# Performance work log

Hardware: AMD Instinct MI355X
Metric: run time of the kernel (lower is better)

## Reference

```python
import jax, jax.numpy as jnp
import numpy as np
import math

B, T, E, H, QL, SUB = 4, 2048, 64, 8, 6, 64  # batch, win_len, n_embd, n_head, q_len, sub_len


def _row_mask(index, sub_len, win_len):
    log_l = math.ceil(np.log2(sub_len))
    mask = np.zeros(win_len, dtype=np.float32)
    if (win_len // sub_len) * 2 * log_l > index:
        mask[: index + 1] = 1
    else:
        while index >= 0:
            if index - log_l + 1 < 0:
                mask[:index] = 1
                break
            mask[index - log_l + 1 : index + 1] = 1
            for i in range(log_l):
                new_index = index - log_l + 1 - 2 ** i
                if index - new_index <= sub_len and new_index >= 0:
                    mask[new_index] = 1
            index -= sub_len
    return mask


def _log_mask(win_len, sub_len):
    m = np.zeros((win_len, win_len), dtype=np.float32)
    for i in range(win_len):
        m[i] = _row_mask(i, sub_len, win_len)
    return m.reshape(1, 1, win_len, win_len)


def setup_inputs() -> dict:
    key = jax.random.key(0)
    ks = jax.random.split(key, 4)
    x = jax.random.normal(ks[0], (B, T, E), dtype=jnp.float32)
    Wqk = jax.random.normal(ks[1], (2 * H * E, E, QL), dtype=jnp.float32) * 0.02
    bqk = jnp.zeros((2 * H * E,), dtype=jnp.float32)
    Wv = jax.random.normal(ks[2], (E, H * E), dtype=jnp.float32) * 0.02
    bv = jnp.zeros((H * E,), dtype=jnp.float32)
    Wp = jax.random.normal(ks[3], (H * E, E), dtype=jnp.float32) * 0.02
    bp = jnp.zeros((E,), dtype=jnp.float32)
    mask = jnp.asarray(_log_mask(T, SUB).astype(bool))  # [1,1,T,T] bool
    return {"x": x, "Wqk": Wqk, "bqk": bqk, "Wv": Wv, "bv": bv,
            "Wp": Wp, "bp": bp, "mask": mask}


def reference(x, Wqk, bqk, Wv, bv, Wp, bp, mask):
    b, t, e = x.shape
    h = Wv.shape[1] // e
    ql = Wqk.shape[-1]

    # value projection (Conv1D rf=1 == dense)
    value = x @ Wv + bv                              # [B,T,H*E]

    # causal conv1d QK projection: left-pad by q_len-1
    xc = jnp.transpose(x, (0, 2, 1))                 # [B,E,T]
    qk = jax.lax.conv_general_dilated(
        xc, Wqk, window_strides=(1,), padding=[(ql - 1, 0)],
        dimension_numbers=("NCH", "OIH", "NCH"))    # [B,2*H*E,T]
    qk = qk + bqk[None, :, None]
    qk = jnp.transpose(qk, (0, 2, 1))                # [B,T,2*H*E]
    query, key_ = jnp.split(qk, 2, axis=2)

    q = query.reshape(b, t, h, e).transpose(0, 2, 1, 3)   # [B,H,T,E]
    k = key_.reshape(b, t, h, e).transpose(0, 2, 3, 1)    # [B,H,E,T]
    v = value.reshape(b, t, h, e).transpose(0, 2, 1, 3)   # [B,H,T,E]

    pre = jnp.einsum("bhqe,bhek->bhqk", q, k) / jnp.sqrt(jnp.asarray(e, x.dtype))
    m = mask[:, :, :t, :t].astype(pre.dtype)
    pre = pre * m + (-1e9) * (1.0 - m)
    attn_weights = jax.nn.softmax(pre, axis=-1)           # [B,H,T,T]
    # dropout p=0.0 -> identity
    attn = jnp.einsum("bhqk,bhke->bhqe", attn_weights, v)  # [B,H,T,E]
    attn = attn.transpose(0, 2, 1, 3).reshape(b, t, h * e)
    out = attn @ Wp + bp                                  # [B,T,E]
    return out, attn_weights
```

## Files before the change

kernel.cpp:

```cpp
#include <hip/hip_runtime.h>
#include <hip/hip_bf16.h>


typedef __attribute__((ext_vector_type(8))) short bf16x8;
typedef __attribute__((ext_vector_type(4))) float f32x4;
typedef unsigned int uint32;

#define MFMA16(a, b, c) __builtin_amdgcn_mfma_f32_16x16x32_bf16((a), (b), (c), 0, 0, 0)

static __device__ __forceinline__ bool sparse_pred(int r, int c) {
  int d = r - c;
  if (d < 0) return false;
  int o = d & 63;
  int j = c + o;
  bool inS = (o <= 7) || (o == 9) || (o == 13) || (o == 21) || (o == 37);
  return (j >= 5) ? inS : (o >= 1);
}

static __device__ __forceinline__ uint32 bfbits(float x) {
  __hip_bfloat16 h = __float2bfloat16(x);
  unsigned short u;
  __builtin_memcpy(&u, &h, 2);
  return (uint32)u;
}

static __device__ __forceinline__ unsigned pred4(bool causal, int ct, int rt, int q, int nt,
                                                 int lq, const unsigned* pm4) {
  const int tb = ct * 64 + 16 * nt + 4 * lq;
  const int thr = q - tb;
  const unsigned cb = (thr < 0) ? 0u : (thr >= 3 ? 0xFu : (0xFu >> (3 - thr)));
  if (causal) return (ct < rt) ? 0xFu : cb;
  if (ct == 0) {
    unsigned p = 0;
#pragma unroll
    for (int reg = 0; reg < 4; ++reg) p |= (unsigned)sparse_pred(q, tb + reg) << reg;
    return p;
  }
  unsigned p = pm4[nt];
  if (ct == rt) p &= cb;
  return p;
}

struct KF {
  bf16x8 a[8];
};

static __device__ __forceinline__ KF loadK(const __hip_bfloat16* __restrict__ kbh, int ct, int lm,
                                           int lq) {
  KF f;
  const __hip_bfloat16* kbase = kbh + (size_t)ct * 64 * 64;
#pragma unroll
  for (int nb = 0; nb < 4; ++nb) {
    const __hip_bfloat16* krow = kbase + (size_t)(16 * nb + lm) * 64;
    f.a[2 * nb] = *reinterpret_cast<const bf16x8*>(krow + lq * 8);
    f.a[2 * nb + 1] = *reinterpret_cast<const bf16x8*>(krow + 32 + lq * 8);
  }
  return f;
}

struct VF {
  bf16x8 a[8];
};

static __device__ __forceinline__ VF loadV(const __hip_bfloat16* __restrict__ vbh, int ct, int lm,
                                           int lq) {
  VF f;
  const __hip_bfloat16* vbase = vbh + ct * 64;
#pragma unroll
  for (int eb = 0; eb < 4; ++eb) {
    const __hip_bfloat16* vrow = vbase + (size_t)(16 * eb + lm) * 2048;
    f.a[2 * eb] = *reinterpret_cast<const bf16x8*>(vrow + lq * 8);
    f.a[2 * eb + 1] = *reinterpret_cast<const bf16x8*>(vrow + 32 + lq * 8);
  }
  return f;
}

__global__ void prep_kernel(const float* __restrict__ Wqk, const float* __restrict__ Wv,
                            __hip_bfloat16* __restrict__ Wt_qk, __hip_bfloat16* __restrict__ Wv_t) {
  int idx = blockIdx.x * 256 + threadIdx.x;
  if (idx < 1024 * 384) {
    int o = idx / 384, kidx = idx - o * 384;
    int kk = kidx >> 6, i = kidx & 63;
    Wt_qk[idx] = __float2bfloat16(Wqk[(o * 64 + i) * 6 + kk]);
  } else {
    int j = idx - 1024 * 384;
    int n = j >> 6, k = j & 63;
    Wv_t[j] = __float2bfloat16(Wv[k * 512 + n]);
  }
}

__global__ __launch_bounds__(256, 4) void proj_kernel(
    const float* __restrict__ x, const float* __restrict__ bqk, const float* __restrict__ bv,
    const __hip_bfloat16* __restrict__ Wt_qk, const __hip_bfloat16* __restrict__ Wv_t,
    __hip_bfloat16* __restrict__ q_bf, __hip_bfloat16* __restrict__ k_bf,
    __hip_bfloat16* __restrict__ v_bf) {
  const int tokTile = blockIdx.x;
  const int chTile = blockIdx.y;
  const int gt0 = tokTile * 64;
  const int b = gt0 >> 11;
  const int t0 = gt0 & 2047;
  const int thr = threadIdx.x;
  __shared__ __align__(16) __hip_bfloat16 xwin[69][72];
  __shared__ __align__(16) __hip_bfloat16 vt[64][72];

  for (int u = thr; u < 69 * 64; u += 256) {
    int row = u >> 6, i = u & 63;
    int t = t0 - 5 + row;
    float v = (t >= 0) ? x[((size_t)b * 2048 + t) * 64 + i] : 0.f;
    xwin[row][i] = __float2bfloat16(v);
  }
  __syncthreads();

  const int wave = thr >> 6, lane = thr & 63;
  const int lm = lane & 15, lq = lane >> 4;
  f32x4 acc[4];
#pragma unroll
  for (int nb = 0; nb < 4; ++nb) acc[nb] = (f32x4){0.f, 0.f, 0.f, 0.f};

  if (chTile < 16) {
    const int ch0 = chTile * 64;
    for (int kc = 0; kc < 12; ++kc) {
      int k0 = kc * 32 + lq * 8;
      int kk = k0 >> 6, i0 = k0 & 63;
      bf16x8 a = *reinterpret_cast<const bf16x8*>(&xwin[16 * wave + lm + kk][i0]);
#pragma unroll
      for (int nb = 0; nb < 4; ++nb) {
        bf16x8 bb =
            *reinterpret_cast<const bf16x8*>(&Wt_qk[(size_t)(ch0 + 16 * nb + lm) * 384 + k0]);
        acc[nb] = MFMA16(a, bb, acc[nb]);
      }
    }
#pragma unroll
    for (int nb = 0; nb < 4; ++nb) {
      int e = 16 * nb + lm;
      float bias = bqk[chTile * 64 + e];
#pragma unroll
      for (int reg = 0; reg < 4; ++reg)
        vt[16 * wave + lq * 4 + reg][e] = __float2bfloat16(acc[nb][reg] + bias);
    }
    __syncthreads();
    const int half = (chTile >> 3) & 1;
    const int h = chTile & 7;
    __hip_bfloat16* dst = half ? k_bf : q_bf;
    for (int u = thr; u < 512; u += 256) {
      int row = u >> 3, c8 = u & 7;
      *reinterpret_cast<uint4*>(dst + ((size_t)((b * 8 + h) * 2048 + t0 + row)) * 64 + c8 * 8) =
          *reinterpret_cast<const uint4*>(&vt[row][c8 * 8]);
    }
  } else {
    const int nv0 = (chTile - 16) * 64;
    for (int kc = 0; kc < 2; ++kc) {
      int i0 = kc * 32 + lq * 8;
      bf16x8 a = *reinterpret_cast<const bf16x8*>(&xwin[16 * wave + lm + 5][i0]);
#pragma unroll
      for (int nb = 0; nb < 4; ++nb) {
        bf16x8 bb = *reinterpret_cast<const bf16x8*>(&Wv_t[(size_t)(nv0 + 16 * nb + lm) * 64 + i0]);
        acc[nb] = MFMA16(a, bb, acc[nb]);
      }
    }
#pragma unroll
    for (int nb = 0; nb < 4; ++nb) {
      int e = 16 * nb + lm;
      float bias = bv[nv0 + e];
#pragma unroll
      for (int reg = 0; reg < 4; ++reg)
        vt[e][16 * wave + lq * 4 + reg] = __float2bfloat16(acc[nb][reg] + bias);
    }
    __syncthreads();
    const int h = chTile - 16;
    for (int u = thr; u < 512; u += 256) {
      int e = u >> 3, c8 = u & 7;
      *reinterpret_cast<uint4*>(v_bf + ((size_t)((b * 8 + h) * 64 + e)) * 2048 + t0 + c8 * 8) =
          *reinterpret_cast<const uint4*>(&vt[e][c8 * 8]);
    }
  }
}

__global__ __launch_bounds__(256, 2) void attn_kernel(
    const __hip_bfloat16* __restrict__ q_bf, const __hip_bfloat16* __restrict__ k_bf,
    const __hip_bfloat16* __restrict__ v_bf,
    float* __restrict__ attn, float* __restrict__ attnout) {
  const int bh = blockIdx.y;
  const int wave = threadIdx.x >> 6;
  const int lane = threadIdx.x & 63;
  const int lm = lane & 15, lq = lane >> 4;

  __shared__ __align__(16) __hip_bfloat16 psw[4][16 * 72];
  __hip_bfloat16* pw = psw[wave];

  const int b2 = bh >> 3, h = bh & 7;
  const __hip_bfloat16* kbh = k_bf + (size_t)bh * 2048 * 64;
  const __hip_bfloat16* vbh = v_bf + (size_t)bh * 64 * 2048;

  const int q64 = 16 * wave + lm;
  unsigned pm4[4];
  {
    const int S[12] = {0, 1, 2, 3, 4, 5, 6, 7, 9, 13, 21, 37};
    unsigned long long M = 0;
#pragma unroll
    for (int i = 0; i < 12; ++i) M |= 1ull << ((q64 - S[i]) & 63);
#pragma unroll
    for (int nt = 0; nt < 4; ++nt) pm4[nt] = (unsigned)((M >> (16 * nt + 4 * lq)) & 0xFull);
  }

  for (int task = 0; task < 2; ++task) {
    const int rt = (task == 0) ? (int)blockIdx.x : 31 - (int)blockIdx.x;
    const int r0 = rt * 64;
    const bool causal = (rt < 6);
    const int q = r0 + q64;

    const __hip_bfloat16* qrow = q_bf + ((size_t)bh * 2048 + q) * 64;
    bf16x8 qa0 = *reinterpret_cast<const bf16x8*>(qrow + lq * 8);
    bf16x8 qa1 = *reinterpret_cast<const bf16x8*>(qrow + 32 + lq * 8);

    float lsum = 0.f;
    {
      KF kc = loadK(kbh, 0, lm, lq);
      for (int ct = 0; ct <= rt; ++ct) {
        KF kn = kc;
        if (ct < rt) kn = loadK(kbh, ct + 1, lm, lq);
#pragma unroll
        for (int nt = 0; nt < 4; ++nt) {
          f32x4 c = (f32x4){0.f, 0.f, 0.f, 0.f};
          c = MFMA16(kc.a[2 * nt], qa0, c);
          c = MFMA16(kc.a[2 * nt + 1], qa1, c);
          const unsigned p = pred4(causal, ct, rt, q, nt, lq, pm4);
#pragma unroll
          for (int reg = 0; reg < 4; ++reg)
            lsum += ((p >> reg) & 1u) ? __expf(c[reg] * 0.125f) : 0.f;
        }
        kc = kn;
      }
    }
    lsum += __shfl_xor(lsum, 16);
    lsum += __shfl_xor(lsum, 32);
    const float inv = 1.f / lsum;

    f32x4 oacc[4];
#pragma unroll
    for (int eb = 0; eb < 4; ++eb) oacc[eb] = (f32x4){0.f, 0.f, 0.f, 0.f};
    float* aq = attn + ((size_t)bh * 2048 + q) * 2048;

    KF kc = loadK(kbh, 0, lm, lq);
    for (int ct = 0; ct <= rt; ++ct) {
      VF vf = loadV(vbh, ct, lm, lq);
      KF kn = kc;
      if (ct < rt) kn = loadK(kbh, ct + 1, lm, lq);
#pragma unroll
      for (int nt = 0; nt < 4; ++nt) {
        f32x4 c = (f32x4){0.f, 0.f, 0.f, 0.f};
        c = MFMA16(kc.a[2 * nt], qa0, c);
        c = MFMA16(kc.a[2 * nt + 1], qa1, c);
        const unsigned p = pred4(causal, ct, rt, q, nt, lq, pm4);
        f32x4 w;
#pragma unroll
        for (int reg = 0; reg < 4; ++reg)
          w[reg] = ((p >> reg) & 1u) ? __expf(c[reg] * 0.125f) * inv : 0.f;
        *reinterpret_cast<f32x4*>(aq + ct * 64 + 16 * nt + 4 * lq) = w;
        uint32 u0 = bfbits(w[0]) | (bfbits(w[1]) << 16);
        uint32 u1 = bfbits(w[2]) | (bfbits(w[3]) << 16);
        uint2 uu = {u0, u1};
        *reinterpret_cast<uint2*>(&pw[lm * 72 + 16 * nt + 4 * lq]) = uu;
      }
      bf16x8 pa0 = *reinterpret_cast<const bf16x8*>(&pw[lm * 72 + lq * 8]);
      bf16x8 pa1 = *reinterpret_cast<const bf16x8*>(&pw[lm * 72 + 32 + lq * 8]);
#pragma unroll
      for (int eb = 0; eb < 4; ++eb) {
        oacc[eb] = MFMA16(vf.a[2 * eb], pa0, oacc[eb]);
        oacc[eb] = MFMA16(vf.a[2 * eb + 1], pa1, oacc[eb]);
      }
      kc = kn;
    }

    float* oq = attnout + ((size_t)(b2 * 2048 + q)) * 512 + h * 64;
#pragma unroll
    for (int eb = 0; eb < 4; ++eb)
      *reinterpret_cast<f32x4*>(oq + 16 * eb + 4 * lq) = oacc[eb];
  }
}

__global__ __launch_bounds__(256, 4) void outproj_kernel(const float* __restrict__ attnout,
                                                         const float* __restrict__ Wp,
                                                         const float* __restrict__ bp,
                                                         float* __restrict__ out) {
  __shared__ __align__(16) float wp_s[128][64];
  const int thr = threadIdx.x;
  const int wave = thr >> 6, lane = thr & 63;
  const int row0 = blockIdx.x * 16 + wave * 4;
  float acc[4] = {0.f, 0.f, 0.f, 0.f};
  for (int kt = 0; kt < 4; ++kt) {
    __syncthreads();
    for (int u = thr; u < 2048; u += 256) {
      int r = u >> 4, c4 = (u & 15) * 4;
      *reinterpret_cast<float4*>(&wp_s[r][c4]) =
          *reinterpret_cast<const float4*>(&Wp[(size_t)(kt * 128 + r) * 64 + c4]);
    }
    __syncthreads();
    for (int k4 = 0; k4 < 32; ++k4) {
      float wv0 = wp_s[k4 * 4 + 0][lane];
      float wv1 = wp_s[k4 * 4 + 1][lane];
      float wv2 = wp_s[k4 * 4 + 2][lane];
      float wv3 = wp_s[k4 * 4 + 3][lane];
#pragma unroll
      for (int rr = 0; rr < 4; ++rr) {
        const float4 a = *reinterpret_cast<const float4*>(
            &attnout[(size_t)(row0 + rr) * 512 + kt * 128 + k4 * 4]);
        acc[rr] += a.x * wv0 + a.y * wv1 + a.z * wv2 + a.w * wv3;
      }
    }
  }
  const float bias = bp[lane];
#pragma unroll
  for (int rr = 0; rr < 4; ++rr) out[(size_t)(row0 + rr) * 64 + lane] = acc[rr] + bias;
}

extern "C" void kernel_launch(void* const* d_in, const int* in_sizes, int n_in, void* d_out,
                              int out_size, void* d_ws, size_t ws_size, hipStream_t stream) {
  (void)in_sizes;
  (void)n_in;
  (void)out_size;
  (void)ws_size;
  const float* x = (const float*)d_in[0];
  const float* Wqk = (const float*)d_in[1];
  const float* bqk = (const float*)d_in[2];
  const float* Wv = (const float*)d_in[3];
  const float* bv = (const float*)d_in[4];
  const float* Wp = (const float*)d_in[5];
  const float* bp = (const float*)d_in[6];

  float* out = (float*)d_out;
  float* attn = out + (size_t)4 * 2048 * 64;

  char* ws = (char*)d_ws;
  __hip_bfloat16* q_bf = (__hip_bfloat16*)(ws);
  __hip_bfloat16* k_bf = (__hip_bfloat16*)(ws + (size_t)8 * 1024 * 1024);
  __hip_bfloat16* v_bf = (__hip_bfloat16*)(ws + (size_t)16 * 1024 * 1024);
  float* attnout = (float*)(ws + (size_t)24 * 1024 * 1024);
  __hip_bfloat16* Wt_qk = (__hip_bfloat16*)(ws + (size_t)40 * 1024 * 1024);
  __hip_bfloat16* Wv_t = (__hip_bfloat16*)(ws + (size_t)41 * 1024 * 1024);

  hipLaunchKernelGGL(prep_kernel, dim3(1664), dim3(256), 0, stream, Wqk, Wv, Wt_qk, Wv_t);
  hipLaunchKernelGGL(proj_kernel, dim3(128, 24), dim3(256), 0, stream, x, bqk, bv, Wt_qk, Wv_t,
                     q_bf, k_bf, v_bf);
  hipLaunchKernelGGL(attn_kernel, dim3(16, 32), dim3(256), 0, stream, q_bf, k_bf, v_bf, attn,
                     attnout);
  hipLaunchKernelGGL(outproj_kernel, dim3(512), dim3(256), 0, stream, attnout, Wp, bp, out);
}
```

Baseline: 754.3 us.

## Split attention key-tile loop across two wave groups with LDS reduction

Result: slower. 866.7 us (+14.9%).

```diff
diff --git a/kernel.cpp b/kernel.cpp
--- a/kernel.cpp
+++ b/kernel.cpp
@@ -176,23 +176,28 @@
   }
 }
 
-__global__ __launch_bounds__(256, 2) void attn_kernel(
+__global__ __launch_bounds__(512, 4) void attn_kernel(
     const __hip_bfloat16* __restrict__ q_bf, const __hip_bfloat16* __restrict__ k_bf,
     const __hip_bfloat16* __restrict__ v_bf,
     float* __restrict__ attn, float* __restrict__ attnout) {
   const int bh = blockIdx.y;
-  const int wave = threadIdx.x >> 6;
-  const int lane = threadIdx.x & 63;
+  const int tid = threadIdx.x;
+  const int wave = tid >> 6;
+  const int band = wave & 3;
+  const int par = wave >> 2;
+  const int lane = tid & 63;
   const int lm = lane & 15, lq = lane >> 4;
 
-  __shared__ __align__(16) __hip_bfloat16 psw[4][16 * 72];
+  __shared__ __align__(16) __hip_bfloat16 psw[8][16 * 72];
+  __shared__ __align__(16) float oxch[2][4][64 * 16];
+  __shared__ float lsx[2][8][16];
   __hip_bfloat16* pw = psw[wave];
 
   const int b2 = bh >> 3, h = bh & 7;
   const __hip_bfloat16* kbh = k_bf + (size_t)bh * 2048 * 64;
   const __hip_bfloat16* vbh = v_bf + (size_t)bh * 64 * 2048;
 
-  const int q64 = 16 * wave + lm;
+  const int q64 = 16 * band + lm;
   unsigned pm4[4];
   {
     const int S[12] = {0, 1, 2, 3, 4, 5, 6, 7, 9, 13, 21, 37};
@@ -214,11 +219,11 @@
     bf16x8 qa1 = *reinterpret_cast<const bf16x8*>(qrow + 32 + lq * 8);
 
     float lsum = 0.f;
-    {
-      KF kc = loadK(kbh, 0, lm, lq);
-      for (int ct = 0; ct <= rt; ++ct) {
+    if (par <= rt) {
+      KF kc = loadK(kbh, par, lm, lq);
+      for (int ct = par; ct <= rt; ct += 2) {
         KF kn = kc;
-        if (ct < rt) kn = loadK(kbh, ct + 1, lm, lq);
+        if (ct + 2 <= rt) kn = loadK(kbh, ct + 2, lm, lq);
 #pragma unroll
         for (int nt = 0; nt < 4; ++nt) {
           f32x4 c = (f32x4){0.f, 0.f, 0.f, 0.f};
@@ -234,48 +239,66 @@
     }
     lsum += __shfl_xor(lsum, 16);
     lsum += __shfl_xor(lsum, 32);
-    const float inv = 1.f / lsum;
+    if (lq == 0) lsx[task][wave][lm] = lsum;
+    __syncthreads();
+    const float inv = 1.f / (lsum + lsx[task][wave ^ 4][lm]);
 
     f32x4 oacc[4];
 #pragma unroll
     for (int eb = 0; eb < 4; ++eb) oacc[eb] = (f32x4){0.f, 0.f, 0.f, 0.f};
     float* aq = attn + ((size_t)bh * 2048 + q) * 2048;
 
-    KF kc = loadK(kbh, 0, lm, lq);
-    for (int ct = 0; ct <= rt; ++ct) {
-      VF vf = loadV(vbh, ct, lm, lq);
-      KF kn = kc;
-      if (ct < rt) kn = loadK(kbh, ct + 1, lm, lq);
-#pragma unroll
-      for (int nt = 0; nt < 4; ++nt) {
-        f32x4 c = (f32x4){0.f, 0.f, 0.f, 0.f};
-        c = MFMA16(kc.a[2 * nt], qa0, c);
-        c = MFMA16(kc.a[2 * nt + 1], qa1, c);
-        const unsigned p = pred4(causal, ct, rt, q, nt, lq, pm4);
-        f32x4 w;
+    if (par <= rt) {
+      KF kc = loadK(kbh, par, lm, lq);
+      for (int ct = par; ct <= rt; ct += 2) {
+        VF vf = loadV(vbh, ct, lm, lq);
+        KF kn = kc;
+        if (ct + 2 <= rt) kn = loadK(kbh, ct + 2, lm, lq);
+#pragma unroll
+        for (int nt = 0; nt < 4; ++nt) {
+          f32x4 c = (f32x4){0.f, 0.f, 0.f, 0.f};
+          c = MFMA16(kc.a[2 * nt], qa0, c);
+          c = MFMA16(kc.a[2 * nt + 1], qa1, c);
+          const unsigned p = pred4(causal, ct, rt, q, nt, lq, pm4);
+          f32x4 w;
+#pragma unroll
+          for (int reg = 0; reg < 4; ++reg)
+            w[reg] = ((p >> reg) & 1u) ? __expf(c[reg] * 0.125f) * inv : 0.f;
+          *reinterpret_cast<f32x4*>(aq + ct * 64 + 16 * nt + 4 * lq) = w;
+          uint32 u0 = bfbits(w[0]) | (bfbits(w[1]) << 16);
+          uint32 u1 = bfbits(w[2]) | (bfbits(w[3]) << 16);
+          uint2 uu = {u0, u1};
+          *reinterpret_cast<uint2*>(&pw[lm * 72 + 16 * nt + 4 * lq]) = uu;
+        }
+        bf16x8 pa0 = *reinterpret_cast<const bf16x8*>(&pw[lm * 72 + lq * 8]);
+        bf16x8 pa1 = *reinterpret_cast<const bf16x8*>(&pw[lm * 72 + 32 + lq * 8]);
+#pragma unroll
+        for (int eb = 0; eb < 4; ++eb) {
+          oacc[eb] = MFMA16(vf.a[2 * eb], pa0, oacc[eb]);
+          oacc[eb] = MFMA16(vf.a[2 * eb + 1], pa1, oacc[eb]);
+        }
+        kc = kn;
+      }
+    }
+
+    if (par == 1) {
+#pragma unroll
+      for (int eb = 0; eb < 4; ++eb)
 #pragma unroll
         for (int reg = 0; reg < 4; ++reg)
-          w[reg] = ((p >> reg) & 1u) ? __expf(c[reg] * 0.125f) * inv : 0.f;
-        *reinterpret_cast<f32x4*>(aq + ct * 64 + 16 * nt + 4 * lq) = w;
-        uint32 u0 = bfbits(w[0]) | (bfbits(w[1]) << 16);
-        uint32 u1 = bfbits(w[2]) | (bfbits(w[3]) << 16);
-        uint2 uu = {u0, u1};
-        *reinterpret_cast<uint2*>(&pw[lm * 72 + 16 * nt + 4 * lq]) = uu;
-      }
-      bf16x8 pa0 = *reinterpret_cast<const bf16x8*>(&pw[lm * 72 + lq * 8]);
-      bf16x8 pa1 = *reinterpret_cast<const bf16x8*>(&pw[lm * 72 + 32 + lq * 8]);
+          oxch[task][band][(16 * eb + 4 * lq + reg) * 16 + lm] = oacc[eb][reg];
+    }
+    __syncthreads();
+    if (par == 0) {
+      float* oq = attnout + ((size_t)(b2 * 2048 + q)) * 512 + h * 64;
 #pragma unroll
       for (int eb = 0; eb < 4; ++eb) {
-        oacc[eb] = MFMA16(vf.a[2 * eb], pa0, oacc[eb]);
-        oacc[eb] = MFMA16(vf.a[2 * eb + 1], pa1, oacc[eb]);
-      }
-      kc = kn;
-    }
-
-    float* oq = attnout + ((size_t)(b2 * 2048 + q)) * 512 + h * 64;
-#pragma unroll
-    for (int eb = 0; eb < 4; ++eb)
-      *reinterpret_cast<f32x4*>(oq + 16 * eb + 4 * lq) = oacc[eb];
+#pragma unroll
+        for (int reg = 0; reg < 4; ++reg)
+          oacc[eb][reg] += oxch[task][band][(16 * eb + 4 * lq + reg) * 16 + lm];
+        *reinterpret_cast<f32x4*>(oq + 16 * eb + 4 * lq) = oacc[eb];
+      }
+    }
   }
 }
 
@@ -342,7 +365,7 @@
   hipLaunchKernelGGL(prep_kernel, dim3(1664), dim3(256), 0, stream, Wqk, Wv, Wt_qk, Wv_t);
   hipLaunchKernelGGL(proj_kernel, dim3(128, 24), dim3(256), 0, stream, x, bqk, bv, Wt_qk, Wv_t,
                      q_bf, k_bf, v_bf);
-  hipLaunchKernelGGL(attn_kernel, dim3(16, 32), dim3(256), 0, stream, q_bf, k_bf, v_bf, attn,
+  hipLaunchKernelGGL(attn_kernel, dim3(16, 32), dim3(512), 0, stream, q_bf, k_bf, v_bf, attn,
                      attnout);
   hipLaunchKernelGGL(outproj_kernel, dim3(512), dim3(256), 0, stream, attnout, Wp, bp, out);
 }
```

## Replace two-pass softmax with single pass and deferred row normalization

Applied to the files above, without the earlier changes.

After: 836.5 us. 10.9% more time.

```diff
diff --git a/kernel.cpp b/kernel.cpp
--- a/kernel.cpp
+++ b/kernel.cpp
@@ -185,8 +185,8 @@
   const int lane = threadIdx.x & 63;
   const int lm = lane & 15, lq = lane >> 4;
 
-  __shared__ __align__(16) __hip_bfloat16 psw[4][16 * 72];
-  __hip_bfloat16* pw = psw[wave];
+  __shared__ __align__(16) __hip_bfloat16 psw[4][2][16 * 72];
+  __shared__ float lsxinv[4][16];
 
   const int b2 = bh >> 3, h = bh & 7;
   const __hip_bfloat16* kbh = k_bf + (size_t)bh * 2048 * 64;
@@ -214,28 +214,6 @@
     bf16x8 qa1 = *reinterpret_cast<const bf16x8*>(qrow + 32 + lq * 8);
 
     float lsum = 0.f;
-    {
-      KF kc = loadK(kbh, 0, lm, lq);
-      for (int ct = 0; ct <= rt; ++ct) {
-        KF kn = kc;
-        if (ct < rt) kn = loadK(kbh, ct + 1, lm, lq);
-#pragma unroll
-        for (int nt = 0; nt < 4; ++nt) {
-          f32x4 c = (f32x4){0.f, 0.f, 0.f, 0.f};
-          c = MFMA16(kc.a[2 * nt], qa0, c);
-          c = MFMA16(kc.a[2 * nt + 1], qa1, c);
-          const unsigned p = pred4(causal, ct, rt, q, nt, lq, pm4);
-#pragma unroll
-          for (int reg = 0; reg < 4; ++reg)
-            lsum += ((p >> reg) & 1u) ? __expf(c[reg] * 0.125f) : 0.f;
-        }
-        kc = kn;
-      }
-    }
-    lsum += __shfl_xor(lsum, 16);
-    lsum += __shfl_xor(lsum, 32);
-    const float inv = 1.f / lsum;
-
     f32x4 oacc[4];
 #pragma unroll
     for (int eb = 0; eb < 4; ++eb) oacc[eb] = (f32x4){0.f, 0.f, 0.f, 0.f};
@@ -246,6 +224,7 @@
       VF vf = loadV(vbh, ct, lm, lq);
       KF kn = kc;
       if (ct < rt) kn = loadK(kbh, ct + 1, lm, lq);
+      __hip_bfloat16* pw = psw[wave][ct & 1];
 #pragma unroll
       for (int nt = 0; nt < 4; ++nt) {
         f32x4 c = (f32x4){0.f, 0.f, 0.f, 0.f};
@@ -255,7 +234,8 @@
         f32x4 w;
 #pragma unroll
         for (int reg = 0; reg < 4; ++reg)
-          w[reg] = ((p >> reg) & 1u) ? __expf(c[reg] * 0.125f) * inv : 0.f;
+          w[reg] = ((p >> reg) & 1u) ? __expf(c[reg] * 0.125f) : 0.f;
+        lsum += w[0] + w[1] + w[2] + w[3];
         *reinterpret_cast<f32x4*>(aq + ct * 64 + 16 * nt + 4 * lq) = w;
         uint32 u0 = bfbits(w[0]) | (bfbits(w[1]) << 16);
         uint32 u1 = bfbits(w[2]) | (bfbits(w[3]) << 16);
@@ -272,10 +252,36 @@
       kc = kn;
     }
 
+    lsum += __shfl_xor(lsum, 16);
+    lsum += __shfl_xor(lsum, 32);
+    const float inv = 1.f / lsum;
+    if (lq == 0) lsxinv[wave][lm] = inv;
+
     float* oq = attnout + ((size_t)(b2 * 2048 + q)) * 512 + h * 64;
 #pragma unroll
-    for (int eb = 0; eb < 4; ++eb)
-      *reinterpret_cast<f32x4*>(oq + 16 * eb + 4 * lq) = oacc[eb];
+    for (int eb = 0; eb < 4; ++eb) {
+      f32x4 o = oacc[eb];
+      o[0] *= inv;
+      o[1] *= inv;
+      o[2] *= inv;
+      o[3] *= inv;
+      *reinterpret_cast<f32x4*>(oq + 16 * eb + 4 * lq) = o;
+    }
+
+    asm volatile("s_waitcnt vmcnt(0)" ::: "memory");
+    const int ncol4 = (rt + 1) * 16;
+    for (int i = 0; i < 16; ++i) {
+      const float iv = lsxinv[wave][i];
+      float* rp = attn + ((size_t)bh * 2048 + r0 + 16 * wave + i) * 2048;
+      for (int c4 = lane; c4 < ncol4; c4 += 64) {
+        f32x4 v = *reinterpret_cast<f32x4*>(rp + 4 * c4);
+        v[0] *= iv;
+        v[1] *= iv;
+        v[2] *= iv;
+        v[3] *= iv;
+        *reinterpret_cast<f32x4*>(rp + 4 * c4) = v;
+      }
+    }
   }
 }
 
```
